# Performance work log

Hardware: AMD Instinct MI355X
Metric: run time of the kernel (lower is better)

The kernel has to match this reference:

```python
import jax, jax.numpy as jnp
import numpy as np

N, C, H, W = 4, 256, 64, 64
S = 2          # scale_factor
K = 5          # up_kernel
G = 1          # up_group
CK = 64        # compressed_channels


def conv2d(x, w, b, pad):
    out = jax.lax.conv_general_dilated(
        x, w, window_strides=(1, 1), padding=[(pad, pad), (pad, pad)],
        dimension_numbers=('NCHW', 'OIHW', 'NCHW'))
    return out + b[None, :, None, None]


def pixel_shuffle(x, r):
    n, cr, h, w = x.shape
    c = cr // (r * r)
    return x.reshape(n, c, r, r, h, w).transpose(0, 1, 4, 2, 5, 3).reshape(n, c, h * r, w * r)


def grid_sample_border(img, grid):
    # img [N,C,Hi,Wi], grid [N,Ho,Wo,2] in [-1,1] (x,y); bilinear, border pad, align_corners=True
    n, c, hi, wi = img.shape
    gx = (grid[..., 0] + 1.0) * 0.5 * (wi - 1)
    gy = (grid[..., 1] + 1.0) * 0.5 * (hi - 1)
    gx = jnp.clip(gx, 0.0, wi - 1.0)
    gy = jnp.clip(gy, 0.0, hi - 1.0)
    x0 = jnp.floor(gx).astype(jnp.int32)
    y0 = jnp.floor(gy).astype(jnp.int32)
    x1 = jnp.minimum(x0 + 1, wi - 1)
    y1 = jnp.minimum(y0 + 1, hi - 1)
    wx = (gx - x0)[..., None]
    wy = (gy - y0)[..., None]
    bidx = jnp.arange(n)[:, None, None]
    def gather(yy, xx):
        return img[bidx, :, yy, xx]  # [N,Ho,Wo,C]
    v00 = gather(y0, x0)
    v01 = gather(y0, x1)
    v10 = gather(y1, x0)
    v11 = gather(y1, x1)
    out = (v00 * (1 - wx) * (1 - wy) + v01 * wx * (1 - wy)
           + v10 * (1 - wx) * wy + v11 * wx * wy)
    return out.transpose(0, 3, 1, 2)


def carafe2(features, masks, k, g, up):
    n, c, h, w = features.shape
    cg = c // g
    k2 = k * k
    # masks [N, g*k2, h*up, w*up] -> per-pixel kernels [n,g,h,w,k2,up2]
    m = masks.reshape(n, g, k2, h, up, w, up)
    m = m.transpose(0, 1, 2, 3, 5, 4, 6).reshape(n, g, k2, h, w, up * up)
    kern = m.transpose(0, 1, 3, 4, 2, 5)            # [n,g,h,w,k2,up2]
    f = features.reshape(n, g, cg, h, w)
    p = k // 2
    fp = jnp.pad(f, ((0, 0), (0, 0), (0, 0), (p, p), (p, p)))
    patches = jnp.stack([fp[:, :, :, i:i + h, j:j + w]
                         for i in range(k) for j in range(k)], axis=-1)  # [n,g,cg,h,w,k2]
    xp = patches.transpose(0, 1, 3, 4, 2, 5)        # [n,g,h,w,cg,k2]
    out = jnp.einsum('nghwck,nghwku->nghwcu', xp, kern)  # [n,g,h,w,cg,up2]
    out = out.transpose(0, 1, 4, 2, 3, 5).reshape(n, c * up * up, h, w)
    return pixel_shuffle(out, up)


def setup_inputs() -> dict:
    key = jax.random.key(0)
    ks = jax.random.split(key, 4)
    x = jax.random.normal(ks[0], (N, C, H, W), dtype=jnp.float32)
    w_comp = jax.random.normal(ks[1], (CK, C, 1, 1), dtype=jnp.float32) * 0.05
    b_comp = jnp.zeros((CK,), dtype=jnp.float32)
    w_ker = jax.random.normal(ks[2], (G * K * K, CK, 3, 3), dtype=jnp.float32) * 0.001
    b_ker = jnp.zeros((G * K * K,), dtype=jnp.float32)
    w_off = jax.random.normal(ks[3], (G * 2 * S * S, CK, 3, 3), dtype=jnp.float32) * 0.01
    b_off = jnp.zeros((G * 2 * S * S,), dtype=jnp.float32)
    return {'x': x, 'w_comp': w_comp, 'b_comp': b_comp,
            'w_ker': w_ker, 'b_ker': b_ker, 'w_off': w_off, 'b_off': b_off}


def reference(x, w_comp, b_comp, w_ker, b_ker, w_off, b_off):
    cx = conv2d(x, w_comp, b_comp, 0)               # channel compressor (1x1)
    offset = conv2d(cx, w_off, b_off, 1)            # [N, 2*S*S, H, W]
    mask = conv2d(cx, w_ker, b_ker, 1)              # [N, G*K*K, H, W]
    # kernel_space_normalizer: softmax over the K*K kernel positions
    n, mc, h, w = mask.shape
    mask = jax.nn.softmax(mask.reshape(n, mc // (K * K), K * K, h, w), axis=2)
    mask = mask.reshape(n, mc, h, w)
    # kernel_space_expander
    off = pixel_shuffle(offset, S).transpose(0, 2, 3, 1)  # [N, H*S, W*S, 2]
    off = off * jnp.array([2.0 / (w - 1), 2.0 / (h - 1)], dtype=off.dtype)
    gh = jnp.repeat(jnp.linspace(-1.0, 1.0, h), S)  # [H*S]
    gw = jnp.repeat(jnp.linspace(-1.0, 1.0, w), S)  # [W*S]
    base = jnp.stack(jnp.broadcast_arrays(gw[None, :], gh[:, None]), axis=-1)  # [H*S, W*S, 2]
    grid = base[None] + off
    mask_ = grid_sample_border(mask, grid)          # [N, G*K*K, H*S, W*S]
    return carafe2(x, mask_, K, G, S)
```

## Files before the change

### kernel.cpp

```cpp
#include <hip/hip_runtime.h>
#include <math.h>

#define NB 4
#define C_IN 256
#define CKC 64
#define HWSZ 4096
#define K2 25
#define NOC2 40

#define WS_CX    0
#define WS_OFF   (WS_CX + NB*CKC*HWSZ)
#define WS_MASK  (WS_OFF + NB*8*HWSZ)
#define WS_WT    (WS_MASK + NB*K2*HWSZ)

#define NWT (CKC * 9 * NOC2)
#define NWC (C_IN * CKC)

__global__ void k_wt(const float* __restrict__ wk, const float* __restrict__ wo,
                     const float* __restrict__ wc,
                     float* __restrict__ wT, float* __restrict__ wcT) {
  int i = blockIdx.x * 256 + threadIdx.x;
  if (i < NWT) {
    int oc = i % NOC2;
    int r = i / NOC2;
    int tap = r % 9, c = r / 9;
    float v = 0.f;
    if (oc < 8)       v = wo[(oc * CKC + c) * 9 + tap];
    else if (oc < 33) v = wk[((oc - 8) * CKC + c) * 9 + tap];
    wT[i] = v;
  } else {
    int j = i - NWT;
    if (j < NWC) {
      int c = j >> 6, ck = j & 63;
      wcT[j] = wc[ck * C_IN + c];
    }
  }
}

__global__ __launch_bounds__(512) void k_compress(const float* __restrict__ x,
    const float* __restrict__ wcT, const float* __restrict__ bc,
    float* __restrict__ cx) {
  __shared__ float s_x[64 * 64];
  int t = threadIdx.x;
  int pos0 = blockIdx.x * 64;
  int n = pos0 >> 12, hw0 = pos0 & 4095;
  int p = t & 63;
  int g = __builtin_amdgcn_readfirstlane(t >> 6);
  const float* xn = x + (size_t)n * (C_IN * HWSZ) + hw0;
  float acc[8];
  #pragma unroll
  for (int i = 0; i < 8; i++) acc[i] = bc[g * 8 + i];

  float rv[8];
  #pragma unroll
  for (int it = 0; it < 8; it++) {
    int idx = t + it * 512;
    int c = idx >> 6, pp = idx & 63;
    rv[it] = xn[c * HWSZ + pp];
  }

  for (int cc = 0; cc < 4; cc++) {
    __syncthreads();
    #pragma unroll
    for (int it = 0; it < 8; it++) s_x[t + it * 512] = rv[it];
    __syncthreads();
    if (cc < 3) {
      #pragma unroll
      for (int it = 0; it < 8; it++) {
        int idx = t + it * 512;
        int c = idx >> 6, pp = idx & 63;
        rv[it] = xn[((cc + 1) * 64 + c) * HWSZ + pp];
      }
    }
    const float* wbase = wcT + (cc * 64) * 64 + g * 8;
    #pragma unroll 4
    for (int c = 0; c < 64; c++) {
      float v = s_x[c * 64 + p];
      const float* w = wbase + c * 64;
      #pragma unroll
      for (int i = 0; i < 8; i++) acc[i] += v * w[i];
    }
  }
  float* o = cx + (size_t)n * (CKC * HWSZ) + hw0 + p;
  #pragma unroll
  for (int i = 0; i < 8; i++) o[(g * 8 + i) * HWSZ] = acc[i];
}

__global__ __launch_bounds__(512) void k_convsm(const float* __restrict__ cx,
    const float* __restrict__ wT, const float* __restrict__ bk, const float* __restrict__ bo,
    float* __restrict__ offb, float* __restrict__ maskb) {
  __shared__ float s_tile[64 * 108];
  __shared__ float s_res[NOC2 * 64];
  int t = threadIdx.x;
  int n = blockIdx.y;
  int tile = blockIdx.x;
  int x0 = (tile & 3) * 16, y0 = (tile >> 2) * 4;
  const float* cxn = cx + n * (CKC * HWSZ);

  for (int idx = t; idx < 6912; idx += 512) {
    int c = idx / 108;
    int rem = idx - c * 108;
    int row = rem / 18, col = rem - row * 18;
    int gy = y0 - 1 + row, gx = x0 - 1 + col;
    float v = 0.f;
    if ((unsigned)gy < 64u && (unsigned)gx < 64u) v = cxn[c * HWSZ + gy * 64 + gx];
    s_tile[idx] = v;
  }
  __syncthreads();

  int p = t & 63;
  int px = p & 15, py = p >> 4;
  int g = __builtin_amdgcn_readfirstlane(t >> 6);
  float acc[5];
  #pragma unroll
  for (int j = 0; j < 5; j++) acc[j] = 0.f;
  const float* wg = wT + g * 5;
  const float* tl0 = s_tile + py * 18 + px;

#define LOADWIN(dst, cidx)                                   \
  {                                                          \
    const float* tlc = tl0 + (cidx) * 108;                   \
    _Pragma("unroll")                                        \
    for (int tap = 0; tap < 9; tap++) {                      \
      int dy = tap / 3, dx = tap % 3;                        \
      dst[tap] = tlc[dy * 18 + dx];                          \
    }                                                        \
  }
#define FMAWIN(src, cidx)                                    \
  {                                                          \
    const float* wc9 = wg + (cidx) * 9 * NOC2;               \
    _Pragma("unroll")                                        \
    for (int tap = 0; tap < 9; tap++) {                      \
      float v = src[tap];                                    \
      const float* w = wc9 + tap * NOC2;                     \
      _Pragma("unroll")                                      \
      for (int j = 0; j < 5; j++) acc[j] += v * w[j];        \
    }                                                        \
  }

  float wa[9], wb[9];
  LOADWIN(wa, 0)
  LOADWIN(wb, 1)
  #pragma unroll 1
  for (int c = 0; c < CKC; c += 2) {
    FMAWIN(wa, c)
    if (c + 2 < CKC) LOADWIN(wa, c + 2)
    FMAWIN(wb, c + 1)
    if (c + 3 < CKC) LOADWIN(wb, c + 3)
  }
#undef LOADWIN
#undef FMAWIN

  #pragma unroll
  for (int j = 0; j < 5; j++) s_res[(g * 5 + j) * 64 + p] = acc[j];
  __syncthreads();

  int hw = (y0 + py) * 64 + x0 + px;
  offb[(n * 8 + g) * HWSZ + hw] = s_res[g * 64 + p] + bo[g];
  if (t < 64) {
    float m[25], mx = -1e30f;
    #pragma unroll
    for (int k = 0; k < 25; k++) { m[k] = s_res[(8 + k) * 64 + p] + bk[k]; mx = fmaxf(mx, m[k]); }
    float s = 0.f;
    #pragma unroll
    for (int k = 0; k < 25; k++) { m[k] = __expf(m[k] - mx); s += m[k]; }
    float inv = 1.f / s;
    #pragma unroll
    for (int k = 0; k < 25; k++) maskb[(n * 25 + k) * HWSZ + hw] = m[k] * inv;
  }
}

__global__ __launch_bounds__(256, 4) void k_carafe(const float* __restrict__ x,
    const float* __restrict__ offb, const float* __restrict__ maskb,
    float* __restrict__ out) {
  __attribute__((aligned(16))) __shared__ float s_patch[32 * 202];
  __attribute__((aligned(16))) __shared__ float s_kern[32 * 25 * 4];
  int t = threadIdx.x;
  int b = blockIdx.x;
  int n = b >> 8;
  int r = b & 255;
  int half = r & 1;
  int wq = (r >> 1) & 3;
  int aa = r >> 3;
  int a = aa + (aa & 16);
  int yout = (a & 15) * 8 + wq * 2 + ((a >> 5) & 1);
  int w0 = wq * 16;
  int cbase = n * C_IN + half * 128;

  int srcOff[13];
  int dstOff[13];
  unsigned vbits = 0;
  unsigned wbits = 0;
  #pragma unroll
  for (int it = 0; it < 13; it++) {
    int e = t + it * 256;
    int c = e / 100;
    int rem = e - c * 100;
    int rg = rem / 10;
    int c2 = rem - rg * 10;
    int row = (rg < 5) ? (a - 2 + rg) : (a + 9 + rg);
    int gc0 = w0 - 2 + c2 * 2;
    bool wr = (e < 3200);
    bool ok = wr & ((unsigned)row < 64u) & ((unsigned)gc0 < 64u);
    srcOff[it] = ok ? (c * HWSZ + row * 64 + gc0) : 0;
    dstOff[it] = wr ? 2 * (e + c) : 0;
    vbits |= (ok ? 1u : 0u) << it;
    wbits |= (wr ? 1u : 0u) << it;
  }

  float2 rv[13];
  {
    const float* xn = x + (size_t)cbase * HWSZ;
    #pragma unroll
    for (int it = 0; it < 13; it++) rv[it] = *(const float2*)(xn + srcOff[it]);
  }

  if (t < 128) {
    int p = t >> 2, u = t & 3;
    int hb = p >> 4, wl = p & 15;
    int h = a + hb * 16;
    int wcol = w0 + wl;
    float ox = offb[(n * 8 + u) * HWSZ + h * 64 + wcol];
    float oy = offb[(n * 8 + 4 + u) * HWSZ + h * 64 + wcol];
    float gx = fminf(fmaxf((float)wcol + ox, 0.f), 63.f);
    float gy = fminf(fmaxf((float)h + oy, 0.f), 63.f);
    float fx0 = floorf(gx), fy0 = floorf(gy);
    int x0 = (int)fx0, y0 = (int)fy0;
    float fx = gx - fx0, fy = gy - fy0;
    int x1 = min(x0 + 1, 63), y1 = min(y0 + 1, 63);
    float w11 = fx * fy;
    float w10 = fy - w11, w01 = fx - w11, w00 = 1.f - fx - fy + w11;
    const float* mb = maskb + n * (K2 * HWSZ);
    int i00 = y0 * 64 + x0, i01 = y0 * 64 + x1;
    int i10 = y1 * 64 + x0, i11 = y1 * 64 + x1;
    #pragma unroll 5
    for (int k = 0; k < 25; k++) {
      const float* mk = mb + k * HWSZ;
      float v = w00 * mk[i00] + w01 * mk[i01] + w10 * mk[i10] + w11 * mk[i11];
      s_kern[(p * 25 + k) * 4 + u] = v;
    }
  }

  int cl = t & 31, g = t >> 5;
  int hb = g >> 2, wl0 = (g & 3) * 4;
  float* s_out = s_patch;

  for (int cc = 0; cc < 4; cc++) {
    __syncthreads();
    #pragma unroll
    for (int it = 0; it < 13; it++) {
      if (wbits & (1u << it)) {
        float2 v = (vbits & (1u << it)) ? rv[it] : make_float2(0.f, 0.f);
        *(float2*)(&s_patch[dstOff[it]]) = v;
      }
    }
    __syncthreads();
    if (cc < 3) {
      const float* xn = x + (size_t)(cbase + (cc + 1) * 32) * HWSZ;
      #pragma unroll
      for (int it = 0; it < 13; it++) rv[it] = *(const float2*)(xn + srcOff[it]);
    }
    float acc[4][4];
    #pragma unroll
    for (int i = 0; i < 4; i++)
      acc[i][0] = acc[i][1] = acc[i][2] = acc[i][3] = 0.f;
    const float* pc = s_patch + cl * 202 + hb * 100 + wl0;
    #pragma unroll
    for (int dy = 0; dy < 5; dy++) {
      float r8[8];
      #pragma unroll
      for (int j = 0; j < 8; j++) r8[j] = pc[dy * 20 + j];
      #pragma unroll
      for (int pr = 0; pr < 4; pr++) {
        const float4* kp = (const float4*)(s_kern + (((g * 4 + pr) * 25) + dy * 5) * 4);
        #pragma unroll
        for (int dx = 0; dx < 5; dx++) {
          float f = r8[pr + dx];
          float4 k4 = kp[dx];
          acc[pr][0] += f * k4.x;
          acc[pr][1] += f * k4.y;
          acc[pr][2] += f * k4.z;
          acc[pr][3] += f * k4.w;
        }
      }
    }
    __syncthreads();
    #pragma unroll
    for (int pr = 0; pr < 4; pr++) {
      int wl = wl0 + pr;
      #pragma unroll
      for (int u = 0; u < 4; u++) {
        int xo = wl * 8 + u * 2 + hb;
        s_out[cl * 130 + xo] = acc[pr][u];
      }
    }
    __syncthreads();
    float* obase = out + ((size_t)(cbase + cc * 32) * 128 + yout) * 128;
    #pragma unroll
    for (int it = 0; it < 4; it++) {
      int q2 = t + it * 256;
      int rowc = q2 >> 5;
      int col4 = q2 & 31;
      const float* sp = s_out + rowc * 130 + col4 * 4;
      float4 v = make_float4(sp[0], sp[1], sp[2], sp[3]);
      *(float4*)(obase + (size_t)rowc * (128 * 128) + col4 * 4) = v;
    }
  }
}

extern "C" void kernel_launch(void* const* d_in, const int* in_sizes, int n_in,
                              void* d_out, int out_size, void* d_ws, size_t ws_size,
                              hipStream_t stream) {
  const float* x      = (const float*)d_in[0];
  const float* w_comp = (const float*)d_in[1];
  const float* b_comp = (const float*)d_in[2];
  const float* w_ker  = (const float*)d_in[3];
  const float* b_ker  = (const float*)d_in[4];
  const float* w_off  = (const float*)d_in[5];
  const float* b_off  = (const float*)d_in[6];
  float* out = (float*)d_out;
  float* ws = (float*)d_ws;
  float* cx    = ws + WS_CX;
  float* offb  = ws + WS_OFF;
  float* maskb = ws + WS_MASK;
  float* wT    = ws + WS_WT;
  float* wcT   = ws + WS_MASK;

  hipLaunchKernelGGL(k_wt, dim3((NWT + NWC + 255) / 256), dim3(256), 0, stream,
                     w_ker, w_off, w_comp, wT, wcT);
  hipLaunchKernelGGL(k_compress, dim3(256), dim3(512), 0, stream, x, wcT, b_comp, cx);
  hipLaunchKernelGGL(k_convsm, dim3(64, 4), dim3(512), 0, stream,
                     cx, wT, b_ker, b_off, offb, maskb);
  hipLaunchKernelGGL(k_carafe, dim3(1024), dim3(256), 0, stream, x, offb, maskb, out);
}
```

Baseline: 181.2 us.

## Fuse 1x1 channel compressor into 3x3 offset/mask conv kernel

Merges the compressor kernel into the conv+softmax kernel. Each block now loads its 18x6 haloed input tile straight from x, computes the 64 compressed channels for that tile in shared memory, then runs the 3x3 conv. This drops the global round trip of the cx intermediate and one launch. In exchange, compressor work is recomputed on halo pixels (108 positions per 64 outputs), padding is handled explicitly, and the block uses more shared memory and registers.

Result: no change. 184.6 us (+1.9%).

```diff
diff --git a/kernel.cpp b/kernel.cpp
--- a/kernel.cpp
+++ b/kernel.cpp
@@ -37,80 +37,77 @@
   }
 }
 
-__global__ __launch_bounds__(512) void k_compress(const float* __restrict__ x,
+__global__ __launch_bounds__(512) void k_cs(const float* __restrict__ x,
     const float* __restrict__ wcT, const float* __restrict__ bc,
-    float* __restrict__ cx) {
-  __shared__ float s_x[64 * 64];
-  int t = threadIdx.x;
-  int pos0 = blockIdx.x * 64;
-  int n = pos0 >> 12, hw0 = pos0 & 4095;
-  int p = t & 63;
-  int g = __builtin_amdgcn_readfirstlane(t >> 6);
-  const float* xn = x + (size_t)n * (C_IN * HWSZ) + hw0;
-  float acc[8];
-  #pragma unroll
-  for (int i = 0; i < 8; i++) acc[i] = bc[g * 8 + i];
-
-  float rv[8];
-  #pragma unroll
-  for (int it = 0; it < 8; it++) {
-    int idx = t + it * 512;
-    int c = idx >> 6, pp = idx & 63;
-    rv[it] = xn[c * HWSZ + pp];
-  }
-
-  for (int cc = 0; cc < 4; cc++) {
-    __syncthreads();
-    #pragma unroll
-    for (int it = 0; it < 8; it++) s_x[t + it * 512] = rv[it];
-    __syncthreads();
-    if (cc < 3) {
-      #pragma unroll
-      for (int it = 0; it < 8; it++) {
-        int idx = t + it * 512;
-        int c = idx >> 6, pp = idx & 63;
-        rv[it] = xn[((cc + 1) * 64 + c) * HWSZ + pp];
-      }
-    }
-    const float* wbase = wcT + (cc * 64) * 64 + g * 8;
-    #pragma unroll 4
-    for (int c = 0; c < 64; c++) {
-      float v = s_x[c * 64 + p];
-      const float* w = wbase + c * 64;
-      #pragma unroll
-      for (int i = 0; i < 8; i++) acc[i] += v * w[i];
-    }
-  }
-  float* o = cx + (size_t)n * (CKC * HWSZ) + hw0 + p;
-  #pragma unroll
-  for (int i = 0; i < 8; i++) o[(g * 8 + i) * HWSZ] = acc[i];
-}
-
-__global__ __launch_bounds__(512) void k_convsm(const float* __restrict__ cx,
     const float* __restrict__ wT, const float* __restrict__ bk, const float* __restrict__ bo,
     float* __restrict__ offb, float* __restrict__ maskb) {
+  __shared__ float s_x[64 * 108];
   __shared__ float s_tile[64 * 108];
-  __shared__ float s_res[NOC2 * 64];
+  float* s_res = s_x;
+
   int t = threadIdx.x;
   int n = blockIdx.y;
   int tile = blockIdx.x;
   int x0 = (tile & 3) * 16, y0 = (tile >> 2) * 4;
-  const float* cxn = cx + n * (CKC * HWSZ);
-
-  for (int idx = t; idx < 6912; idx += 512) {
+  const float* xn = x + (size_t)n * (C_IN * HWSZ);
+
+  int srcOff[14];
+  unsigned vb = 0, wb = 0;
+  #pragma unroll
+  for (int it = 0; it < 14; it++) {
+    int idx = t + it * 512;
     int c = idx / 108;
     int rem = idx - c * 108;
     int row = rem / 18, col = rem - row * 18;
     int gy = y0 - 1 + row, gx = x0 - 1 + col;
-    float v = 0.f;
-    if ((unsigned)gy < 64u && (unsigned)gx < 64u) v = cxn[c * HWSZ + gy * 64 + gx];
-    s_tile[idx] = v;
+    bool wr = (idx < 6912);
+    bool ok = wr & ((unsigned)gy < 64u) & ((unsigned)gx < 64u);
+    srcOff[it] = ok ? (c * HWSZ + gy * 64 + gx) : 0;
+    vb |= (ok ? 1u : 0u) << it;
+    wb |= (wr ? 1u : 0u) << it;
+  }
+  float rv[14];
+  #pragma unroll
+  for (int it = 0; it < 14; it++) rv[it] = xn[srcOff[it]];
+
+  int p = t & 63;
+  int g = __builtin_amdgcn_readfirstlane(t >> 6);
+  int pos1 = p + 64;
+  int pos1c = (pos1 < 108) ? pos1 : 107;
+  float a0[8], a1[8];
+  #pragma unroll
+  for (int i = 0; i < 8; i++) { a0[i] = bc[g * 8 + i]; a1[i] = a0[i]; }
+
+  for (int cc = 0; cc < 4; cc++) {
+    __syncthreads();
+    #pragma unroll
+    for (int it = 0; it < 14; it++)
+      if (wb & (1u << it)) s_x[t + it * 512] = (vb & (1u << it)) ? rv[it] : 0.f;
+    __syncthreads();
+    if (cc < 3) {
+      const float* xb = xn + (size_t)(cc + 1) * 64 * HWSZ;
+      #pragma unroll
+      for (int it = 0; it < 14; it++) rv[it] = xb[srcOff[it]];
+    }
+    const float* wbase = wcT + (cc * 64) * 64 + g * 8;
+    #pragma unroll 4
+    for (int c = 0; c < 64; c++) {
+      float v0 = s_x[c * 108 + p];
+      float v1 = s_x[c * 108 + pos1c];
+      const float* w = wbase + c * 64;
+      #pragma unroll
+      for (int i = 0; i < 8; i++) { a0[i] += v0 * w[i]; a1[i] += v1 * w[i]; }
+    }
+  }
+  #pragma unroll
+  for (int i = 0; i < 8; i++) s_tile[(g * 8 + i) * 108 + p] = a0[i];
+  if (pos1 < 108) {
+    #pragma unroll
+    for (int i = 0; i < 8; i++) s_tile[(g * 8 + i) * 108 + pos1] = a1[i];
   }
   __syncthreads();
 
-  int p = t & 63;
   int px = p & 15, py = p >> 4;
-  int g = __builtin_amdgcn_readfirstlane(t >> 6);
   float acc[5];
   #pragma unroll
   for (int j = 0; j < 5; j++) acc[j] = 0.f;
@@ -138,15 +135,15 @@
     }                                                        \
   }
 
-  float wa[9], wb[9];
+  float wa[9], wbuf[9];
   LOADWIN(wa, 0)
-  LOADWIN(wb, 1)
+  LOADWIN(wbuf, 1)
   #pragma unroll 1
   for (int c = 0; c < CKC; c += 2) {
     FMAWIN(wa, c)
     if (c + 2 < CKC) LOADWIN(wa, c + 2)
-    FMAWIN(wb, c + 1)
-    if (c + 3 < CKC) LOADWIN(wb, c + 3)
+    FMAWIN(wbuf, c + 1)
+    if (c + 3 < CKC) LOADWIN(wbuf, c + 3)
   }
 #undef LOADWIN
 #undef FMAWIN
@@ -320,16 +317,14 @@
   const float* b_off  = (const float*)d_in[6];
   float* out = (float*)d_out;
   float* ws = (float*)d_ws;
-  float* cx    = ws + WS_CX;
   float* offb  = ws + WS_OFF;
   float* maskb = ws + WS_MASK;
   float* wT    = ws + WS_WT;
-  float* wcT   = ws + WS_MASK;
+  float* wcT   = ws + WS_CX;
 
   hipLaunchKernelGGL(k_wt, dim3((NWT + NWC + 255) / 256), dim3(256), 0, stream,
                      w_ker, w_off, w_comp, wT, wcT);
-  hipLaunchKernelGGL(k_compress, dim3(256), dim3(512), 0, stream, x, wcT, b_comp, cx);
-  hipLaunchKernelGGL(k_convsm, dim3(64, 4), dim3(512), 0, stream,
-                     cx, wT, b_ker, b_off, offb, maskb);
+  hipLaunchKernelGGL(k_cs, dim3(64, 4), dim3(512), 0, stream,
+                     x, wcT, b_comp, wT, b_ker, b_off, offb, maskb);
   hipLaunchKernelGGL(k_carafe, dim3(1024), dim3(256), 0, stream, x, offb, maskb, out);
 }
```
